# Performance work log

Hardware: AMD Instinct MI355X
Metric: run time of the kernel (lower is better)

Reference implementation:

```python
import jax, jax.numpy as jnp
import numpy as np
import math

N = 100000      # num nodes
D = 5           # fixed degree per node (<=5 -> exact Shapley enumeration path)
F_IN = 128
F_OUT = 128


def _subset_coeffs(d):
    """Exact Shapley subset-enumeration coefficients for a node with d neighbors.
    For subset S (mask m_k over neighbor slots, |S|=s):
      marginal = (sum_S + x_i)/(s+1) - (sum_S/s if s>0 else 0)   [since mean_S]
      weight   = s! (d-s)! / (d+1)!
    contrib = sum_k w_k*marginal_k = einsum(sum_S, c1) + x_i * sum(c2)
    """
    k = np.arange(2 ** d)
    masks = ((k[:, None] >> np.arange(d)) & 1).astype(np.float32)  # [2^d, d]
    s = masks.sum(axis=1)
    fact = np.vectorize(math.factorial)
    w = (fact(s.astype(np.int64)) * fact((d - s).astype(np.int64))
         / math.factorial(d + 1)).astype(np.float32)
    c1 = np.where(s > 0, w * (1.0 / (s + 1.0) - 1.0 / np.maximum(s, 1.0)), 0.0).astype(np.float32)
    c2 = (w / (s + 1.0)).astype(np.float32)
    return jnp.asarray(masks), jnp.asarray(c1), jnp.asarray(float(c2.sum()))


def setup_inputs() -> dict:
    key = jax.random.key(0)
    k1, k2, k3 = jax.random.split(key, 3)
    x = jax.random.normal(k1, (N, F_IN), dtype=jnp.float32)
    # fixed-degree graph: node i owns edges [i*D, (i+1)*D); row sorted
    row = jnp.repeat(jnp.arange(N, dtype=jnp.int32), D)
    col = jax.random.randint(k2, (N * D,), 0, N, dtype=jnp.int32)
    edge_index = jnp.stack([row, col])  # [2, N*D]
    W = jax.random.normal(k3, (F_OUT, F_IN), dtype=jnp.float32) / np.float32(np.sqrt(F_IN))
    return {"x": x, "edge_index": edge_index, "W": W}


def reference(x, edge_index, W):
    n = x.shape[0]
    col = edge_index[1]
    d = col.shape[0] // n
    nbrs = col.reshape(n, d)          # neighbors of node i (row is sorted, fixed degree)
    xn = x[nbrs]                      # [n, d, f] gathered neighbor features
    masks, c1, c2_sum = _subset_coeffs(d)
    # per-subset neighbor-feature sums: [n, 2^d, f]
    sum_S = jnp.einsum('kd,ndf->nkf', masks, xn)
    contrib = jnp.einsum('nkf,k->nf', sum_S, c1) + x * c2_sum
    shapley = x + contrib             # x_i + Shapley contribution
    out = jax.nn.relu(shapley @ W.T)  # Linear(bias=False) + relu
    return out
```

## Files before the change

kernel.cpp:

```cpp
#include <hip/hip_runtime.h>
#include <hip/hip_bf16.h>

typedef __attribute__((ext_vector_type(8))) short short8;
typedef __attribute__((ext_vector_type(4))) float f32x4;

#define DEG 5
#define FDIM 128
#define NTHR 256
#define LROW 136

#define CSELF 1.4083333333333334f
#define ALPHA (-0.04833333333333333f)

__device__ __forceinline__ short f2bf(float f) {
    unsigned u = __builtin_bit_cast(unsigned, f);
    unsigned r = (u + 0x7fffu + ((u >> 16) & 1u)) >> 16;
    return (short)(r & 0xffffu);
}
__device__ __forceinline__ float bf2f(short s) {
    return __builtin_bit_cast(float, (unsigned)((unsigned short)s) << 16);
}

__global__ __launch_bounds__(256) void prep_w_kernel(
    const float* __restrict__ W, short* __restrict__ wswz)
{
    int t = blockIdx.x * 256 + threadIdx.x;
    int frag = t >> 6;
    int lane = t & 63;
    int tt = frag >> 2;
    int kk = frag & 3;
    int lr = lane & 15;
    int lg = lane >> 4;
    const float4* wp = reinterpret_cast<const float4*>(W + (tt * 16 + lr) * FDIM + kk * 32 + lg * 8);
    float4 w0 = wp[0], w1 = wp[1];
    short8 v;
    v[0] = f2bf(w0.x); v[1] = f2bf(w0.y); v[2] = f2bf(w0.z); v[3] = f2bf(w0.w);
    v[4] = f2bf(w1.x); v[5] = f2bf(w1.y); v[6] = f2bf(w1.z); v[7] = f2bf(w1.w);
    *reinterpret_cast<short8*>(wswz + (size_t)t * 8) = v;
}

__global__ __launch_bounds__(256) void conv_xb_kernel(
    const float* __restrict__ x, short* __restrict__ xb, long total8)
{
    long t = (long)blockIdx.x * 256 + threadIdx.x;
    if (t < total8) {
        const f32x4* xp = reinterpret_cast<const f32x4*>(x + t * 8);
        f32x4 a = xp[0], b = xp[1];
        short8 v;
        v[0] = f2bf(a[0]); v[1] = f2bf(a[1]); v[2] = f2bf(a[2]); v[3] = f2bf(a[3]);
        v[4] = f2bf(b[0]); v[5] = f2bf(b[1]); v[6] = f2bf(b[2]); v[7] = f2bf(b[3]);
        *reinterpret_cast<short8*>(xb + t * 8) = v;
    }
}

__global__ __launch_bounds__(NTHR) void shapley_gather_kernel(
    const short* __restrict__ xb,
    const int* __restrict__ col,
    const short* __restrict__ wswz,
    float* __restrict__ out,
    int n)
{
    const int tid = threadIdx.x;
    const int wave = tid >> 6;
    const int lane = tid & 63;
    const int r = lane & 15;
    const int h = lane >> 4;

    const int grp = blockIdx.x * 4 + wave;
    const int node = grp * 16 + r;
    const int nc = node < n ? node : 0;

    int idx[DEG];
    #pragma unroll
    for (int j = 0; j < DEG; ++j) idx[j] = col[nc * DEG + j];

    short8 self[4];
    short8 nb[DEG][4];
    {
        const short* sp = xb + (size_t)nc * FDIM + h * 8;
        #pragma unroll
        for (int kk = 0; kk < 4; ++kk)
            self[kk] = *reinterpret_cast<const short8*>(sp + kk * 32);
        #pragma unroll
        for (int j = 0; j < DEG; ++j) {
            const short* np = xb + (size_t)idx[j] * FDIM + h * 8;
            #pragma unroll
            for (int kk = 0; kk < 4; ++kk)
                nb[j][kk] = *reinterpret_cast<const short8*>(np + kk * 32);
        }
    }
    __builtin_amdgcn_sched_barrier(0);

    short8 af[4];
    #pragma unroll
    for (int kk = 0; kk < 4; ++kk) {
        #pragma unroll
        for (int e = 0; e < 8; ++e) {
            float s = bf2f(nb[0][kk][e]) + bf2f(nb[1][kk][e]) + bf2f(nb[2][kk][e])
                    + bf2f(nb[3][kk][e]) + bf2f(nb[4][kk][e]);
            float v = CSELF * bf2f(self[kk][e]) + ALPHA * s;
            af[kk][e] = f2bf(v);
        }
    }

    f32x4 acc[8];
    #pragma unroll
    for (int q = 0; q < 8; ++q) acc[q] = (f32x4){0.f, 0.f, 0.f, 0.f};

    #pragma unroll
    for (int q = 0; q < 8; ++q) {
        #pragma unroll
        for (int kk = 0; kk < 4; ++kk) {
            short8 bf = *reinterpret_cast<const short8*>(
                wswz + (((size_t)(q * 4 + kk) * 64 + lane) * 8));
            acc[q] = __builtin_amdgcn_mfma_f32_16x16x32_bf16(af[kk], bf, acc[q], 0, 0, 0);
        }
    }

    #pragma unroll
    for (int q = 0; q < 8; ++q) {
        #pragma unroll
        for (int i = 0; i < 4; ++i) {
            int orow = grp * 16 + h * 4 + i;
            if (orow < n) {
                float v = acc[q][i];
                out[(size_t)orow * FDIM + q * 16 + r] = v > 0.f ? v : 0.f;
            }
        }
    }
}

__global__ __launch_bounds__(NTHR) void shapley_fb_kernel(
    const float* __restrict__ x,
    const int* __restrict__ col,
    const short* __restrict__ wswz,
    float* __restrict__ out,
    int n)
{
    __shared__ short sS[64 * LROW];
    __shared__ int sIdx[64 * DEG];

    const int tid = threadIdx.x;
    const int base = blockIdx.x * 64;

    for (int i = tid; i < 64 * DEG; i += NTHR) {
        int e = base * DEG + i;
        sIdx[i] = (e < n * DEG) ? col[e] : 0;
    }
    __syncthreads();

    for (int t = tid; t < 64 * 16; t += NTHR) {
        int m = t >> 4;
        int c = t & 15;
        int node = base + m;
        float a0, a1, a2, a3, a4, a5, a6, a7;
        if (node < n) {
            const float4* xp = reinterpret_cast<const float4*>(x + (size_t)node * FDIM + c * 8);
            float4 s0 = xp[0], s1 = xp[1];
            a0 = CSELF * s0.x; a1 = CSELF * s0.y; a2 = CSELF * s0.z; a3 = CSELF * s0.w;
            a4 = CSELF * s1.x; a5 = CSELF * s1.y; a6 = CSELF * s1.z; a7 = CSELF * s1.w;
            #pragma unroll
            for (int j = 0; j < DEG; ++j) {
                int nb = sIdx[m * DEG + j];
                const float4* np = reinterpret_cast<const float4*>(x + (size_t)nb * FDIM + c * 8);
                float4 b0 = np[0], b1 = np[1];
                a0 += ALPHA * b0.x; a1 += ALPHA * b0.y; a2 += ALPHA * b0.z; a3 += ALPHA * b0.w;
                a4 += ALPHA * b1.x; a5 += ALPHA * b1.y; a6 += ALPHA * b1.z; a7 += ALPHA * b1.w;
            }
        } else {
            a0 = a1 = a2 = a3 = a4 = a5 = a6 = a7 = 0.f;
        }
        short8 v;
        v[0] = f2bf(a0); v[1] = f2bf(a1); v[2] = f2bf(a2); v[3] = f2bf(a3);
        v[4] = f2bf(a4); v[5] = f2bf(a5); v[6] = f2bf(a6); v[7] = f2bf(a7);
        *reinterpret_cast<short8*>(&sS[m * LROW + c * 8]) = v;
    }
    __syncthreads();

    const int wave = tid >> 6;
    const int lane = tid & 63;
    const int lr = lane & 15;
    const int lg = lane >> 4;

    short8 afrag[4];
    const short* arow = &sS[(wave * 16 + lr) * LROW];
    #pragma unroll
    for (int kk = 0; kk < 4; ++kk)
        afrag[kk] = *reinterpret_cast<const short8*>(arow + kk * 32 + lg * 8);

    f32x4 acc[8];
    #pragma unroll
    for (int t = 0; t < 8; ++t) acc[t] = (f32x4){0.f, 0.f, 0.f, 0.f};

    #pragma unroll
    for (int t = 0; t < 8; ++t) {
        #pragma unroll
        for (int kk = 0; kk < 4; ++kk) {
            short8 bfrag = *reinterpret_cast<const short8*>(
                wswz + (((size_t)(t * 4 + kk) * 64 + lane) * 8));
            acc[t] = __builtin_amdgcn_mfma_f32_16x16x32_bf16(afrag[kk], bfrag, acc[t], 0, 0, 0);
        }
    }

    #pragma unroll
    for (int t = 0; t < 8; ++t) {
        #pragma unroll
        for (int i = 0; i < 4; ++i) {
            int nrow = base + wave * 16 + lg * 4 + i;
            if (nrow < n) {
                float v = acc[t][i];
                out[(size_t)nrow * FDIM + t * 16 + lr] = v > 0.f ? v : 0.f;
            }
        }
    }
}

extern "C" void kernel_launch(void* const* d_in, const int* in_sizes, int n_in,
                              void* d_out, int out_size, void* d_ws, size_t ws_size,
                              hipStream_t stream) {
    const float* x  = (const float*)d_in[0];
    const int* ei   = (const int*)d_in[1];
    const float* W  = (const float*)d_in[2];
    float* out      = (float*)d_out;

    int n = in_sizes[0] / FDIM;
    const int* col = ei + (size_t)n * DEG;

    short* wswz = (short*)d_ws;
    size_t xb_off = 32768;
    size_t need   = xb_off + (size_t)n * FDIM * sizeof(short);

    hipLaunchKernelGGL(prep_w_kernel, dim3(8), dim3(256), 0, stream, W, wswz);

    if (ws_size >= need) {
        short* xb = (short*)((char*)d_ws + xb_off);
        long total8 = (long)n * FDIM / 8;
        int cblocks = (int)((total8 + 255) / 256);
        hipLaunchKernelGGL(conv_xb_kernel, dim3(cblocks), dim3(256), 0, stream,
                           x, xb, total8);
        int groups = (n + 15) / 16;
        int blocks = (groups + 3) / 4;
        hipLaunchKernelGGL(shapley_gather_kernel, dim3(blocks), dim3(NTHR), 0, stream,
                           xb, col, wswz, out, n);
    } else {
        int blocks = (n + 63) / 64;
        hipLaunchKernelGGL(shapley_fb_kernel, dim3(blocks), dim3(NTHR), 0, stream,
                           x, col, wswz, out, n);
    }
}
```

Measured before the change: 61.22 us.

## Gather neighbor rows into LDS via global_load_lds and split MFMA across waves

Replaces the register-based per-lane neighbor gather with direct global-to-LDS asynchronous loads (global_load_lds) for a 32-node tile. The neighbor rows are then combined from LDS, staged as bf16 in shared memory, and the 32x128 GEMM is split over four waves, each handling 16 rows by 64 output columns. The goal is to cut VGPR pressure and improve gather memory-level parallelism. The cost is about 40KB of LDS per block, which limits occupancy, plus extra barriers and LDS traffic.

Result: faster. 57.37 us (-6.3%).

```diff
diff --git a/kernel.cpp b/kernel.cpp
--- a/kernel.cpp
+++ b/kernel.cpp
@@ -6,8 +6,11 @@
 
 #define DEG 5
 #define FDIM 128
+#define MT 32
 #define NTHR 256
 #define LROW 136
+#define NROWS (MT * DEG)
+#define NINSTR (NROWS / 4)
 
 #define CSELF 1.4083333333333334f
 #define ALPHA (-0.04833333333333333f)
@@ -53,78 +56,100 @@
     }
 }
 
-__global__ __launch_bounds__(NTHR) void shapley_gather_kernel(
+__global__ __launch_bounds__(NTHR) void shapley_glds_kernel(
     const short* __restrict__ xb,
     const int* __restrict__ col,
     const short* __restrict__ wswz,
     float* __restrict__ out,
     int n)
 {
+    __shared__ short gbuf[NROWS * FDIM];
+    __shared__ short sS[MT * LROW];
+    __shared__ int sIdx[NROWS];
+
     const int tid = threadIdx.x;
+    const int base = blockIdx.x * MT;
+
+    if (tid < NROWS) {
+        int e = base * DEG + tid;
+        sIdx[tid] = (e < n * DEG) ? col[e] : 0;
+    }
+    __syncthreads();
+
     const int wave = tid >> 6;
     const int lane = tid & 63;
-    const int r = lane & 15;
-    const int h = lane >> 4;
-
-    const int grp = blockIdx.x * 4 + wave;
-    const int node = grp * 16 + r;
-    const int nc = node < n ? node : 0;
-
-    int idx[DEG];
-    #pragma unroll
-    for (int j = 0; j < DEG; ++j) idx[j] = col[nc * DEG + j];
-
-    short8 self[4];
-    short8 nb[DEG][4];
-    {
-        const short* sp = xb + (size_t)nc * FDIM + h * 8;
-        #pragma unroll
-        for (int kk = 0; kk < 4; ++kk)
-            self[kk] = *reinterpret_cast<const short8*>(sp + kk * 32);
-        #pragma unroll
-        for (int j = 0; j < DEG; ++j) {
-            const short* np = xb + (size_t)idx[j] * FDIM + h * 8;
-            #pragma unroll
-            for (int kk = 0; kk < 4; ++kk)
-                nb[j][kk] = *reinterpret_cast<const short8*>(np + kk * 32);
-        }
-    }
-    __builtin_amdgcn_sched_barrier(0);
+
+    for (int i = wave; i < NINSTR; i += 4) {
+        int r = i * 4 + (lane >> 4);
+        int nbr = sIdx[r];
+        const short* gp = xb + (size_t)nbr * FDIM + (lane & 15) * 8;
+        __builtin_amdgcn_global_load_lds(
+            (const __attribute__((address_space(1))) unsigned int*)gp,
+            (__attribute__((address_space(3))) unsigned int*)&gbuf[i * 512],
+            16, 0, 0);
+    }
+    asm volatile("s_waitcnt vmcnt(0)" ::: "memory");
+    __syncthreads();
+
+    const int c = tid & 15;
+    const int s = tid >> 4;
+
+    #pragma unroll
+    for (int u = 0; u < 2; ++u) {
+        int m = u * 16 + s;
+        int node = base + m;
+        int nc = node < n ? node : 0;
+        short8 sv = *reinterpret_cast<const short8*>(xb + (size_t)nc * FDIM + c * 8);
+        short8 nb0 = *reinterpret_cast<const short8*>(&gbuf[(m * DEG + 0) * FDIM + c * 8]);
+        short8 nb1 = *reinterpret_cast<const short8*>(&gbuf[(m * DEG + 1) * FDIM + c * 8]);
+        short8 nb2 = *reinterpret_cast<const short8*>(&gbuf[(m * DEG + 2) * FDIM + c * 8]);
+        short8 nb3 = *reinterpret_cast<const short8*>(&gbuf[(m * DEG + 3) * FDIM + c * 8]);
+        short8 nb4 = *reinterpret_cast<const short8*>(&gbuf[(m * DEG + 4) * FDIM + c * 8]);
+        short8 v;
+        #pragma unroll
+        for (int k = 0; k < 8; ++k) {
+            float sum = bf2f(nb0[k]) + bf2f(nb1[k]) + bf2f(nb2[k])
+                      + bf2f(nb3[k]) + bf2f(nb4[k]);
+            v[k] = f2bf(CSELF * bf2f(sv[k]) + ALPHA * sum);
+        }
+        *reinterpret_cast<short8*>(&sS[m * LROW + c * 8]) = v;
+    }
+    __syncthreads();
+
+    const int lr = lane & 15;
+    const int lg = lane >> 4;
+    const int rt = wave & 1;
+    const int cg = wave >> 1;
 
     short8 af[4];
-    #pragma unroll
-    for (int kk = 0; kk < 4; ++kk) {
-        #pragma unroll
-        for (int e = 0; e < 8; ++e) {
-            float s = bf2f(nb[0][kk][e]) + bf2f(nb[1][kk][e]) + bf2f(nb[2][kk][e])
-                    + bf2f(nb[3][kk][e]) + bf2f(nb[4][kk][e]);
-            float v = CSELF * bf2f(self[kk][e]) + ALPHA * s;
-            af[kk][e] = f2bf(v);
-        }
-    }
-
-    f32x4 acc[8];
-    #pragma unroll
-    for (int q = 0; q < 8; ++q) acc[q] = (f32x4){0.f, 0.f, 0.f, 0.f};
-
-    #pragma unroll
-    for (int q = 0; q < 8; ++q) {
+    const short* arow = &sS[(rt * 16 + lr) * LROW];
+    #pragma unroll
+    for (int kk = 0; kk < 4; ++kk)
+        af[kk] = *reinterpret_cast<const short8*>(arow + kk * 32 + lg * 8);
+
+    f32x4 acc[4];
+    #pragma unroll
+    for (int q = 0; q < 4; ++q) acc[q] = (f32x4){0.f, 0.f, 0.f, 0.f};
+
+    #pragma unroll
+    for (int q = 0; q < 4; ++q) {
+        int tcol = cg * 4 + q;
         #pragma unroll
         for (int kk = 0; kk < 4; ++kk) {
             short8 bf = *reinterpret_cast<const short8*>(
-                wswz + (((size_t)(q * 4 + kk) * 64 + lane) * 8));
+                wswz + (((size_t)(tcol * 4 + kk) * 64 + lane) * 8));
             acc[q] = __builtin_amdgcn_mfma_f32_16x16x32_bf16(af[kk], bf, acc[q], 0, 0, 0);
         }
     }
 
     #pragma unroll
-    for (int q = 0; q < 8; ++q) {
+    for (int q = 0; q < 4; ++q) {
         #pragma unroll
         for (int i = 0; i < 4; ++i) {
-            int orow = grp * 16 + h * 4 + i;
+            int orow = base + rt * 16 + lg * 4 + i;
             if (orow < n) {
                 float v = acc[q][i];
-                out[(size_t)orow * FDIM + q * 16 + r] = v > 0.f ? v : 0.f;
+                out[(size_t)orow * FDIM + (cg * 4 + q) * 16 + lr] = v > 0.f ? v : 0.f;
             }
         }
     }
@@ -238,9 +263,8 @@
         int cblocks = (int)((total8 + 255) / 256);
         hipLaunchKernelGGL(conv_xb_kernel, dim3(cblocks), dim3(256), 0, stream,
                            x, xb, total8);
-        int groups = (n + 15) / 16;
-        int blocks = (groups + 3) / 4;
-        hipLaunchKernelGGL(shapley_gather_kernel, dim3(blocks), dim3(NTHR), 0, stream,
+        int blocks = (n + MT - 1) / MT;
+        hipLaunchKernelGGL(shapley_glds_kernel, dim3(blocks), dim3(NTHR), 0, stream,
                            xb, col, wswz, out, n);
     } else {
         int blocks = (n + 63) / 64;
```
